# Kernel tuning notes

Hardware: AMD Instinct MI355X
Metric: run time of the kernel (lower is better)

## Reference

```python
import jax, jax.numpy as jnp
import numpy as np

N = 384          # item_num (text regions)
TD = 768         # text hidden (bert-base)
VD = 768         # vision hidden (vit-base)
CD = TD + VD     # commu_dim = 1536
FF = 2048        # TransformerEncoderLayer default dim_feedforward
H = 4            # nhead
L = 2            # num_layers per encoder
EPS = 1e-5


def _enc_params(key, d, scale=0.02):
    ks = jax.random.split(key, 6)
    return dict(
        qkv_w=jax.random.normal(ks[0], (L, 3 * d, d), jnp.float32) * scale,
        qkv_b=jnp.zeros((L, 3 * d), jnp.float32),
        out_w=jax.random.normal(ks[1], (L, d, d), jnp.float32) * scale,
        out_b=jnp.zeros((L, d), jnp.float32),
        ln1_s=jnp.ones((L, d), jnp.float32),
        ln1_b=jnp.zeros((L, d), jnp.float32),
        ff1_w=jax.random.normal(ks[2], (L, FF, d), jnp.float32) * scale,
        ff1_b=jnp.zeros((L, FF), jnp.float32),
        ff2_w=jax.random.normal(ks[3], (L, d, FF), jnp.float32) * scale,
        ff2_b=jnp.zeros((L, d), jnp.float32),
        ln2_s=jnp.ones((L, d), jnp.float32),
        ln2_b=jnp.zeros((L, d), jnp.float32),
    )


def setup_inputs() -> dict:
    key = jax.random.key(0)
    k = jax.random.split(key, 6)
    inp = {
        'text_emb': jax.random.normal(k[0], (N, TD), jnp.float32),
        'vision_emb': jax.random.normal(k[1], (N, VD), jnp.float32),
        'gt_matrix': jax.random.randint(k[2], (N, N), 0, 2, jnp.int32),
    }
    for pref, kk, d in (('t_', k[3], TD), ('c_', k[4], CD)):
        for name, v in _enc_params(kk, d).items():
            inp[pref + name] = v
    inp['lin_w'] = jax.random.normal(k[5], (2, 2 * CD), jnp.float32) * 0.02
    inp['lin_b'] = jnp.zeros((2,), jnp.float32)
    return inp


def _ln(x, s, b):
    m = jnp.mean(x, -1, keepdims=True)
    v = jnp.mean((x - m) ** 2, -1, keepdims=True)
    return (x - m) * jax.lax.rsqrt(v + EPS) * s + b


def _encoder(x, qkv_w, qkv_b, out_w, out_b, ln1_s, ln1_b,
             ff1_w, ff1_b, ff2_w, ff2_b, ln2_s, ln2_b):
    # PyTorch post-norm TransformerEncoder, relu activation, eval mode (no dropout)
    d = x.shape[-1]
    hd = d // H
    for l in range(qkv_w.shape[0]):
        qkv = x @ qkv_w[l].T + qkv_b[l]
        q, kk, v = jnp.split(qkv, 3, axis=-1)
        q = q.reshape(-1, H, hd)
        kk = kk.reshape(-1, H, hd)
        v = v.reshape(-1, H, hd)
        scores = jnp.einsum('qhd,khd->hqk', q, kk) / jnp.sqrt(jnp.float32(hd))
        attn = jax.nn.softmax(scores, -1)
        o = jnp.einsum('hqk,khd->qhd', attn, v).reshape(-1, d)
        x = _ln(x + o @ out_w[l].T + out_b[l], ln1_s[l], ln1_b[l])
        h = jax.nn.relu(x @ ff1_w[l].T + ff1_b[l]) @ ff2_w[l].T + ff2_b[l]
        x = _ln(x + h, ln2_s[l], ln2_b[l])
    return x


def reference(text_emb, vision_emb, gt_matrix,
              t_qkv_w, t_qkv_b, t_out_w, t_out_b, t_ln1_s, t_ln1_b,
              t_ff1_w, t_ff1_b, t_ff2_w, t_ff2_b, t_ln2_s, t_ln2_b,
              c_qkv_w, c_qkv_b, c_out_w, c_out_b, c_ln1_s, c_ln1_b,
              c_ff1_w, c_ff1_b, c_ff2_w, c_ff2_b, c_ln2_s, c_ln2_b,
              lin_w, lin_b):
    te = _encoder(text_emb, t_qkv_w, t_qkv_b, t_out_w, t_out_b, t_ln1_s, t_ln1_b,
                  t_ff1_w, t_ff1_b, t_ff2_w, t_ff2_b, t_ln2_s, t_ln2_b)
    all_emb = jnp.concatenate([te, vision_emb], axis=1)  # [N, CD]
    all_emb = _encoder(all_emb, c_qkv_w, c_qkv_b, c_out_w, c_out_b, c_ln1_s, c_ln1_b,
                       c_ff1_w, c_ff1_b, c_ff2_w, c_ff2_b, c_ln2_s, c_ln2_b)
    # organize(): linear(cat(e_i, e_j)) decomposes exactly as e_i@Wa^T + e_j@Wb^T + b,
    # avoiding the O(N^2 * 2*CD) pair tensor while computing identical math.
    a = all_emb @ lin_w[:, :CD].T + lin_b      # [N, 2]
    c = all_emb @ lin_w[:, CD:].T              # [N, 2]
    logits = a[:, None, :] + c[None, :, :]     # [N, N, 2]
    probs = jax.nn.softmax(logits, -1)         # self.activate(self.linear(...))
    # classificaiton_loss: sum_i CrossEntropyLoss(probs[i], gt[i])  (CE takes probs as logits)
    ls = jax.nn.log_softmax(probs, -1)
    cell = -jnp.take_along_axis(ls, gt_matrix[..., None].astype(jnp.int32), axis=-1)[..., 0]
    cls_loss = jnp.sum(jnp.mean(cell, axis=1))
    # enter_exit_loss over first N-1 items
    link = probs[:, :, 1]
    ee_loss = jnp.sum(jnp.abs(link.sum(1)[:-1] + link.sum(0)[:-1] - 1.0))
    return probs, cls_loss, ee_loss
```

## Files before the change

kernel.cpp:

```cpp
#include <hip/hip_runtime.h>
#include <hip/hip_bf16.h>
#include <math.h>

#define NTOK 384
#define HEADS 4

typedef __attribute__((ext_vector_type(8))) short bf16x8;
typedef __attribute__((ext_vector_type(4))) float f32x4;

__device__ __forceinline__ unsigned short f2b(float f) {
    union { float f; unsigned int u; } v; v.f = f;
    unsigned int r = (v.u + 0x7fff + ((v.u >> 16) & 1)) >> 16;
    return (unsigned short)r;
}

__device__ __forceinline__ void g2l16(const void* g, void* l) {
    __builtin_amdgcn_global_load_lds(
        (const __attribute__((address_space(1))) unsigned int*)g,
        (__attribute__((address_space(3))) unsigned int*)l, 16, 0, 0);
}

__device__ __forceinline__ void stage64(
    const unsigned short* __restrict__ g, int row0, int k0, int ld,
    char* region, int wid, int lane)
{
    int c = wid * 64 + lane;
    int row = c >> 2, p = c & 3;
    int kc = (p - (row >> 1)) & 3;
    g2l16(g + (long)(row0 + row) * ld + k0 + kc * 8,
          region + (wid * 64) * 16);
}

__device__ __forceinline__ void stage_tile(
    const unsigned short* __restrict__ A, const unsigned short* __restrict__ B,
    int row0, int col0, int k0, int lda, int ldb,
    char* buf, int wid, int lane)
{
    stage64(A, row0, k0,      lda, buf,         wid, lane);
    stage64(A, row0, k0 + 32, lda, buf +  4096, wid, lane);
    stage64(B, col0, k0,      ldb, buf +  8192, wid, lane);
    stage64(B, col0, k0 + 32, ldb, buf + 12288, wid, lane);
    __builtin_amdgcn_sched_barrier(0);
}

__global__ __launch_bounds__(256, 3) void gemm64(
    const unsigned short* __restrict__ A, const unsigned short* __restrict__ B,
    const float* __restrict__ bias, void* __restrict__ Cv,
    int K, int lda, int ldb, int ldc,
    long sA, long sB, long sC, int relu, int out_bf16)
{
    __shared__ char smem[3][16384];
    A += (long)blockIdx.z * sA;
    B += (long)blockIdx.z * sB;
    const int t = threadIdx.x, lane = t & 63, wid = t >> 6;
    const int wm = wid >> 1, wn = wid & 1;
    const int r16 = lane & 15, quad = lane >> 4;
    const int row0 = blockIdx.y * 64, col0 = blockIdx.x * 64;

    f32x4 acc[2][2] = {};
    const int NT = K >> 6;

    stage_tile(A, B, row0, col0, 0, lda, ldb, smem[0], wid, lane);
    if (NT > 1)
        stage_tile(A, B, row0, col0, 64, lda, ldb, smem[1], wid, lane);

    int cur = 0, sb = 2;
    for (int kt = 0; kt < NT; ++kt) {
        if (kt + 1 < NT) asm volatile("s_waitcnt vmcnt(4)" ::: "memory");
        else             asm volatile("s_waitcnt vmcnt(0) lgkmcnt(0)" ::: "memory");
        __builtin_amdgcn_s_barrier();
        if (kt + 2 < NT) {
            stage_tile(A, B, row0, col0, (kt + 2) * 64, lda, ldb,
                       smem[sb], wid, lane);
            sb = (sb == 2) ? 0 : sb + 1;
        }
        const char* cb = smem[cur];
        cur = (cur == 2) ? 0 : cur + 1;
        #pragma unroll
        for (int h = 0; h < 2; ++h) {
            bf16x8 af[2], bfv[2];
            #pragma unroll
            for (int rt = 0; rt < 2; ++rt) {
                int row = wm * 32 + rt * 16 + r16;
                int p = (quad + (row >> 1)) & 3;
                af[rt] = *reinterpret_cast<const bf16x8*>(
                    cb + h * 4096 + row * 64 + p * 16);
            }
            #pragma unroll
            for (int ct = 0; ct < 2; ++ct) {
                int col = wn * 32 + ct * 16 + r16;
                int p = (quad + (col >> 1)) & 3;
                bfv[ct] = *reinterpret_cast<const bf16x8*>(
                    cb + 8192 + h * 4096 + col * 64 + p * 16);
            }
            #pragma unroll
            for (int rt = 0; rt < 2; ++rt)
                #pragma unroll
                for (int ct = 0; ct < 2; ++ct)
                    acc[rt][ct] = __builtin_amdgcn_mfma_f32_16x16x32_bf16(
                        af[rt], bfv[ct], acc[rt][ct], 0, 0, 0);
        }
    }

    float* Cf = (float*)Cv;
    unsigned short* Cb = (unsigned short*)Cv;
    const long zoff = (long)blockIdx.z * sC;
    #pragma unroll
    for (int rt = 0; rt < 2; ++rt) {
        #pragma unroll
        for (int ct = 0; ct < 2; ++ct) {
            f32x4 v = acc[rt][ct];
            int col = col0 + wn * 32 + ct * 16 + r16;
            float bi = bias ? bias[col] : 0.f;
            #pragma unroll
            for (int i = 0; i < 4; ++i) {
                v[i] += bi;
                if (relu) v[i] = fmaxf(v[i], 0.f);
            }
            int rbase = row0 + wm * 32 + rt * 16 + quad * 4;
            if (out_bf16) {
                #pragma unroll
                for (int i = 0; i < 4; ++i)
                    Cb[zoff + (long)(rbase + i) * ldc + col] = f2b(v[i]);
            } else {
                #pragma unroll
                for (int i = 0; i < 4; ++i)
                    Cf[zoff + (long)(rbase + i) * ldc + col] = v[i];
            }
        }
    }
}

__device__ __forceinline__ void stage128(
    const unsigned short* __restrict__ g, int row0, int k0, int ld,
    char* region, int tid)
{
    int row = tid >> 2, p = tid & 3;
    int kc = (p - (row >> 1)) & 3;
    g2l16(g + (long)(row0 + row) * ld + k0 + kc * 8,
          region + ((tid >> 6) * 64) * 16);
}

__device__ __forceinline__ void stage_tile128(
    const unsigned short* __restrict__ A, const unsigned short* __restrict__ B,
    int row0, int col0, int k0, int lda, int ldb,
    char* buf, int tid)
{
    stage128(A, row0, k0,      lda, buf,          tid);
    stage128(A, row0, k0 + 32, lda, buf +  8192,  tid);
    stage128(B, col0, k0,      ldb, buf + 16384,  tid);
    stage128(B, col0, k0 + 32, ldb, buf + 24576,  tid);
    __builtin_amdgcn_sched_barrier(0);
}

__global__ __launch_bounds__(512, 1) void gemm128(
    const unsigned short* __restrict__ A, const unsigned short* __restrict__ B,
    const float* __restrict__ bias, void* __restrict__ Cv,
    int K, int lda, int ldb, int ldc, int relu, int out_bf16,
    unsigned short* __restrict__ vt, int dv2)
{
    __shared__ char smem[3][32768];
    const int t = threadIdx.x, lane = t & 63, wid = t >> 6;
    const int wm = wid >> 2, wn = wid & 3;
    const int r16 = lane & 15, quad = lane >> 4;
    const int row0 = blockIdx.y * 128, col0 = blockIdx.x * 128;

    f32x4 acc[4][2] = {};
    const int NT = K >> 6;

    stage_tile128(A, B, row0, col0, 0, lda, ldb, smem[0], t);
    if (NT > 1)
        stage_tile128(A, B, row0, col0, 64, lda, ldb, smem[1], t);

    int cur = 0, sb = 2;
    for (int kt = 0; kt < NT; ++kt) {
        if (kt + 1 < NT) asm volatile("s_waitcnt vmcnt(4)" ::: "memory");
        else             asm volatile("s_waitcnt vmcnt(0) lgkmcnt(0)" ::: "memory");
        __builtin_amdgcn_s_barrier();
        if (kt + 2 < NT) {
            stage_tile128(A, B, row0, col0, (kt + 2) * 64, lda, ldb,
                          smem[sb], t);
            sb = (sb == 2) ? 0 : sb + 1;
        }
        const char* cb = smem[cur];
        cur = (cur == 2) ? 0 : cur + 1;
        #pragma unroll
        for (int h = 0; h < 2; ++h) {
            bf16x8 af[4], bfv[2];
            #pragma unroll
            for (int rt = 0; rt < 4; ++rt) {
                int row = wm * 64 + rt * 16 + r16;
                int p = (quad + (row >> 1)) & 3;
                af[rt] = *reinterpret_cast<const bf16x8*>(
                    cb + h * 8192 + row * 64 + p * 16);
            }
            #pragma unroll
            for (int ct = 0; ct < 2; ++ct) {
                int col = wn * 32 + ct * 16 + r16;
                int p = (quad + (col >> 1)) & 3;
                bfv[ct] = *reinterpret_cast<const bf16x8*>(
                    cb + 16384 + h * 8192 + col * 64 + p * 16);
            }
            #pragma unroll
            for (int rt = 0; rt < 4; ++rt)
                #pragma unroll
                for (int ct = 0; ct < 2; ++ct)
                    acc[rt][ct] = __builtin_amdgcn_mfma_f32_16x16x32_bf16(
                        af[rt], bfv[ct], acc[rt][ct], 0, 0, 0);
        }
    }

    float* Cf = (float*)Cv;
    unsigned short* Cb = (unsigned short*)Cv;
    const int vwrite = (vt != nullptr) && (col0 >= dv2);
    #pragma unroll
    for (int rt = 0; rt < 4; ++rt) {
        #pragma unroll
        for (int ct = 0; ct < 2; ++ct) {
            f32x4 v = acc[rt][ct];
            int col = col0 + wn * 32 + ct * 16 + r16;
            float bi = bias ? bias[col] : 0.f;
            #pragma unroll
            for (int i = 0; i < 4; ++i) {
                v[i] += bi;
                if (relu) v[i] = fmaxf(v[i], 0.f);
            }
            int rbase = row0 + wm * 64 + rt * 16 + quad * 4;
            if (vwrite) {
                ushort4 p;
                p.x = f2b(v[0]); p.y = f2b(v[1]); p.z = f2b(v[2]); p.w = f2b(v[3]);
                *reinterpret_cast<ushort4*>(vt + (long)(col - dv2) * NTOK + rbase) = p;
            } else if (out_bf16) {
                #pragma unroll
                for (int i = 0; i < 4; ++i)
                    Cb[(long)(rbase + i) * ldc + col] = f2b(v[i]);
            } else {
                #pragma unroll
                for (int i = 0; i < 4; ++i)
                    Cf[(long)(rbase + i) * ldc + col] = v[i];
            }
        }
    }
}

#define WO0 0u
#define WO1 3538944u
#define WO2 4718592u
#define WO3 7864320u
#define WO4 11010048u
#define WO5 25165824u
#define WO6 29884416u
#define WO7 36175872u
#define WTOT 42467328u

__global__ __launch_bounds__(256) void convert_weights(
    const float* __restrict__ s0, const float* __restrict__ s1,
    const float* __restrict__ s2, const float* __restrict__ s3,
    const float* __restrict__ s4, const float* __restrict__ s5,
    const float* __restrict__ s6, const float* __restrict__ s7,
    unsigned short* __restrict__ dst)
{
    unsigned int e = (blockIdx.x * 256u + threadIdx.x) * 16u;
    if (e >= WTOT) return;
    const float* src; unsigned int local;
    if      (e < WO1) { src = s0; local = e - WO0; }
    else if (e < WO2) { src = s1; local = e - WO1; }
    else if (e < WO3) { src = s2; local = e - WO2; }
    else if (e < WO4) { src = s3; local = e - WO3; }
    else if (e < WO5) { src = s4; local = e - WO4; }
    else if (e < WO6) { src = s5; local = e - WO5; }
    else if (e < WO7) { src = s6; local = e - WO6; }
    else              { src = s7; local = e - WO7; }
    float4 v0 = *reinterpret_cast<const float4*>(src + local);
    float4 v1 = *reinterpret_cast<const float4*>(src + local + 4);
    float4 v2 = *reinterpret_cast<const float4*>(src + local + 8);
    float4 v3 = *reinterpret_cast<const float4*>(src + local + 12);
    uint4 o0, o1;
    o0.x = (unsigned)f2b(v0.x) | ((unsigned)f2b(v0.y) << 16);
    o0.y = (unsigned)f2b(v0.z) | ((unsigned)f2b(v0.w) << 16);
    o0.z = (unsigned)f2b(v1.x) | ((unsigned)f2b(v1.y) << 16);
    o0.w = (unsigned)f2b(v1.z) | ((unsigned)f2b(v1.w) << 16);
    o1.x = (unsigned)f2b(v2.x) | ((unsigned)f2b(v2.y) << 16);
    o1.y = (unsigned)f2b(v2.z) | ((unsigned)f2b(v2.w) << 16);
    o1.z = (unsigned)f2b(v3.x) | ((unsigned)f2b(v3.y) << 16);
    o1.w = (unsigned)f2b(v3.z) | ((unsigned)f2b(v3.w) << 16);
    *reinterpret_cast<uint4*>(dst + e) = o0;
    *reinterpret_cast<uint4*>(dst + e + 8) = o1;
}

__global__ __launch_bounds__(64) void softmax_rows(
    const float* __restrict__ S, unsigned short* __restrict__ P, float scale)
{
    const float* p = S + (long)blockIdx.x * NTOK;
    unsigned short* q = P + (long)blockIdx.x * NTOK;
    const int t = threadIdx.x;
    float vals[6];
    float vmax = -1e30f;
    #pragma unroll
    for (int i = 0; i < 6; ++i) {
        vals[i] = p[t + i * 64] * scale;
        vmax = fmaxf(vmax, vals[i]);
    }
    for (int off = 32; off; off >>= 1) vmax = fmaxf(vmax, __shfl_down(vmax, off));
    vmax = __shfl(vmax, 0);
    float sum = 0.f;
    #pragma unroll
    for (int i = 0; i < 6; ++i) { vals[i] = __expf(vals[i] - vmax); sum += vals[i]; }
    for (int off = 32; off; off >>= 1) sum += __shfl_down(sum, off);
    sum = __shfl(sum, 0);
    float inv = 1.f / sum;
    #pragma unroll
    for (int i = 0; i < 6; ++i) q[t + i * 64] = f2b(vals[i] * inv);
}

__global__ __launch_bounds__(256) void add_ln(
    float* __restrict__ x, unsigned short* __restrict__ xb,
    const float* __restrict__ y,
    const float* __restrict__ gb,
    const float* __restrict__ s, const float* __restrict__ b, int d)
{
    float* xr = x + (long)blockIdx.x * d;
    unsigned short* xbr = xb + (long)blockIdx.x * d;
    const float* yr = y + (long)blockIdx.x * d;
    const int t = threadIdx.x;
    float vv[6];
    float s1 = 0.f, s2 = 0.f;
    #pragma unroll
    for (int j = 0; j < 6; ++j) {
        int i = t + j * 256;
        if (j * 256 < d) {
            float v = xr[i] + gb[i] + yr[i];
            vv[j] = v;
            s1 += v; s2 += v * v;
        }
    }
    for (int off = 32; off; off >>= 1) { s1 += __shfl_down(s1, off); s2 += __shfl_down(s2, off); }
    __shared__ float r1[4], r2[4];
    int w = t >> 6;
    if ((t & 63) == 0) { r1[w] = s1; r2[w] = s2; }
    __syncthreads();
    if (t == 0) {
        float a = 0.f, c = 0.f;
        for (int i = 0; i < 4; ++i) { a += r1[i]; c += r2[i]; }
        r1[0] = a; r2[0] = c;
    }
    __syncthreads();
    float mean = r1[0] / d;
    float var = r2[0] / d - mean * mean;
    float rstd = rsqrtf(var + 1e-5f);
    #pragma unroll
    for (int j = 0; j < 6; ++j) {
        int i = t + j * 256;
        if (j * 256 < d) {
            float v = (vv[j] - mean) * rstd * s[i] + b[i];
            xr[i] = v;
            xbr[i] = f2b(v);
        }
    }
}

__global__ void initx_k(const float* __restrict__ src, float* __restrict__ dst,
                        unsigned short* __restrict__ dstb, int n)
{
    int i = blockIdx.x * blockDim.x + threadIdx.x;
    if (i < n) { float v = src[i]; dst[i] = v; dstb[i] = f2b(v); }
}

__global__ void concat_k(const float* __restrict__ te, const float* __restrict__ ve,
                         float* __restrict__ all, unsigned short* __restrict__ allb)
{
    int i = blockIdx.x * blockDim.x + threadIdx.x;
    if (i >= NTOK * 1536) return;
    int r = i / 1536, c = i % 1536;
    float v = (c < 768) ? te[r * 768 + c] : ve[r * 768 + (c - 768)];
    all[i] = v;
    allb[i] = f2b(v);
}

__global__ __launch_bounds__(256) void head_ac(
    const float* __restrict__ all, const float* __restrict__ lin_w,
    const float* __restrict__ lin_b, float* __restrict__ a, float* __restrict__ c)
{
    const int i = blockIdx.x, t = threadIdx.x;
    const float* xr = all + (long)i * 1536;
    float s0 = 0.f, s1 = 0.f, s2 = 0.f, s3 = 0.f;
    for (int e = t; e < 1536; e += 256) {
        float v = xr[e];
        s0 += v * lin_w[e];
        s1 += v * lin_w[3072 + e];
        s2 += v * lin_w[1536 + e];
        s3 += v * lin_w[4608 + e];
    }
    for (int off = 32; off; off >>= 1) {
        s0 += __shfl_down(s0, off); s1 += __shfl_down(s1, off);
        s2 += __shfl_down(s2, off); s3 += __shfl_down(s3, off);
    }
    __shared__ float r[4][4];
    int w = t >> 6;
    if ((t & 63) == 0) { r[0][w] = s0; r[1][w] = s1; r[2][w] = s2; r[3][w] = s3; }
    __syncthreads();
    if (t == 0) {
        float t0 = 0.f, t1 = 0.f, t2 = 0.f, t3 = 0.f;
        for (int k = 0; k < 4; ++k) { t0 += r[0][k]; t1 += r[1][k]; t2 += r[2][k]; t3 += r[3][k]; }
        a[i * 2 + 0] = t0 + lin_b[0];
        a[i * 2 + 1] = t1 + lin_b[1];
        c[i * 2 + 0] = t2;
        c[i * 2 + 1] = t3;
    }
}

__global__ __launch_bounds__(384) void head_probs(
    const float* __restrict__ a, const float* __restrict__ c,
    const int* __restrict__ gt, float* __restrict__ probs,
    float* __restrict__ rowsum, float* __restrict__ rowcell)
{
    const int i = blockIdx.x, j = threadIdx.x;
    float l0 = a[i * 2 + 0] + c[j * 2 + 0];
    float l1 = a[i * 2 + 1] + c[j * 2 + 1];
    float m = fmaxf(l0, l1);
    float e0 = __expf(l0 - m), e1 = __expf(l1 - m);
    float inv = 1.f / (e0 + e1);
    float p0 = e0 * inv, p1 = e1 * inv;
    long base = ((long)i * NTOK + j) * 2;
    probs[base] = p0;
    probs[base + 1] = p1;
    float m2 = fmaxf(p0, p1);
    float z = m2 + __logf(__expf(p0 - m2) + __expf(p1 - m2));
    int g = gt[i * NTOK + j];
    float cell = z - (g ? p1 : p0);
    float cs = cell, ps = p1;
    for (int off = 32; off; off >>= 1) { cs += __shfl_down(cs, off); ps += __shfl_down(ps, off); }
    __shared__ float rc[6], rs[6];
    int w = j >> 6;
    if ((j & 63) == 0) { rc[w] = cs; rs[w] = ps; }
    __syncthreads();
    if (j == 0) {
        float csum = 0.f, psum = 0.f;
        for (int k = 0; k < 6; ++k) { csum += rc[k]; psum += rs[k]; }
        rowcell[i] = csum * (1.f / NTOK);
        rowsum[i] = psum;
    }
}

__global__ __launch_bounds__(64) void colsum_k(const float* __restrict__ probs,
                                               float* __restrict__ colsum)
{
    const int j = blockIdx.x, t = threadIdx.x;
    float s = 0.f;
    for (int i = t; i < NTOK; i += 64)
        s += probs[((long)i * NTOK + j) * 2 + 1];
    for (int off = 32; off; off >>= 1) s += __shfl_down(s, off);
    if (t == 0) colsum[j] = s;
}

__global__ __launch_bounds__(384) void finalize_k(
    const float* __restrict__ rowcell, const float* __restrict__ rowsum,
    const float* __restrict__ colsum, float* __restrict__ out)
{
    const int t = threadIdx.x;
    float cls = rowcell[t];
    float ee = (t < NTOK - 1) ? fabsf(rowsum[t] + colsum[t] - 1.f) : 0.f;
    for (int off = 32; off; off >>= 1) { cls += __shfl_down(cls, off); ee += __shfl_down(ee, off); }
    __shared__ float rc[6], re[6];
    int w = t >> 6;
    if ((t & 63) == 0) { rc[w] = cls; re[w] = ee; }
    __syncthreads();
    if (t == 0) {
        float a = 0.f, b = 0.f;
        for (int k = 0; k < 6; ++k) { a += rc[k]; b += re[k]; }
        out[NTOK * NTOK * 2 + 0] = a;
        out[NTOK * NTOK * 2 + 1] = b;
    }
}

static void run_encoder(float* x, unsigned short* xb, int d,
                        const unsigned short* wq, const unsigned short* wo,
                        const unsigned short* w1, const unsigned short* w2,
                        const float* qkv_b, const float* out_b,
                        const float* ln1_s, const float* ln1_b,
                        const float* ff1_b, const float* ff2_b,
                        const float* ln2_s, const float* ln2_b,
                        unsigned short* qkvb, float* sc, unsigned short* attnb,
                        unsigned short* vtb, unsigned short* ob,
                        unsigned short* t1b, float* t2,
                        hipStream_t stream)
{
    const int dq = 3 * d;
    const int hd = d / HEADS;
    const float scale = 1.0f / sqrtf((float)hd);
    for (int l = 0; l < 2; ++l) {
        gemm128<<<dim3(dq / 128, NTOK / 128), 512, 0, stream>>>(
            xb, wq + (long)l * dq * d, qkv_b + l * dq, qkvb,
            d, d, d, dq, 0, 1, vtb, 2 * d);
        gemm64<<<dim3(6, 6, HEADS), 256, 0, stream>>>(
            qkvb, qkvb + d, nullptr, sc,
            hd, dq, dq, NTOK, (long)hd, (long)hd, (long)NTOK * NTOK, 0, 0);
        softmax_rows<<<HEADS * NTOK, 64, 0, stream>>>(sc, attnb, scale);
        gemm64<<<dim3(hd / 64, 6, HEADS), 256, 0, stream>>>(
            attnb, vtb, nullptr, ob,
            NTOK, NTOK, NTOK, d, (long)NTOK * NTOK, (long)hd * NTOK, (long)hd,
            0, 1);
        gemm128<<<dim3(d / 128, NTOK / 128), 512, 0, stream>>>(
            ob, wo + (long)l * d * d, nullptr, t2,
            d, d, d, d, 0, 0, nullptr, 0);
        add_ln<<<NTOK, 256, 0, stream>>>(x, xb, t2,
                                         out_b + l * d, ln1_s + l * d, ln1_b + l * d, d);
        gemm128<<<dim3(2048 / 128, NTOK / 128), 512, 0, stream>>>(
            xb, w1 + (long)l * 2048 * d, ff1_b + l * 2048, t1b,
            d, d, d, 2048, 1, 1, nullptr, 0);
        gemm128<<<dim3(d / 128, NTOK / 128), 512, 0, stream>>>(
            t1b, w2 + (long)l * d * 2048, nullptr, t2,
            2048, 2048, 2048, d, 0, 0, nullptr, 0);
        add_ln<<<NTOK, 256, 0, stream>>>(x, xb, t2,
                                         ff2_b + l * d, ln2_s + l * d, ln2_b + l * d, d);
    }
}

extern "C" void kernel_launch(void* const* d_in, const int* in_sizes, int n_in,
                              void* d_out, int out_size, void* d_ws, size_t ws_size,
                              hipStream_t stream)
{
    const float* text_emb   = (const float*)d_in[0];
    const float* vision_emb = (const float*)d_in[1];
    const int*   gt         = (const int*)  d_in[2];
    const float* t_qkv_w = (const float*)d_in[3];
    const float* t_qkv_b = (const float*)d_in[4];
    const float* t_out_w = (const float*)d_in[5];
    const float* t_out_b = (const float*)d_in[6];
    const float* t_ln1_s = (const float*)d_in[7];
    const float* t_ln1_b = (const float*)d_in[8];
    const float* t_ff1_w = (const float*)d_in[9];
    const float* t_ff1_b = (const float*)d_in[10];
    const float* t_ff2_w = (const float*)d_in[11];
    const float* t_ff2_b = (const float*)d_in[12];
    const float* t_ln2_s = (const float*)d_in[13];
    const float* t_ln2_b = (const float*)d_in[14];
    const float* c_qkv_w = (const float*)d_in[15];
    const float* c_qkv_b = (const float*)d_in[16];
    const float* c_out_w = (const float*)d_in[17];
    const float* c_out_b = (const float*)d_in[18];
    const float* c_ln1_s = (const float*)d_in[19];
    const float* c_ln1_b = (const float*)d_in[20];
    const float* c_ff1_w = (const float*)d_in[21];
    const float* c_ff1_b = (const float*)d_in[22];
    const float* c_ff2_w = (const float*)d_in[23];
    const float* c_ff2_b = (const float*)d_in[24];
    const float* c_ln2_s = (const float*)d_in[25];
    const float* c_ln2_b = (const float*)d_in[26];
    const float* lin_w   = (const float*)d_in[27];
    const float* lin_b   = (const float*)d_in[28];
    float* out = (float*)d_out;

    float* ws = (float*)d_ws;
    float* xt      = ws;
    float* all     = xt + 294912;
    float* t2      = all + 589824;
    float* sc      = t2 + 589824;
    float* abuf    = sc + 589824;
    float* cbuf    = abuf + 768;
    float* rowsum  = cbuf + 768;
    float* rowcell = rowsum + 384;
    float* colsum  = rowcell + 384;
    unsigned short* ub = (unsigned short*)(ws + 2067072);
    unsigned short* xtb   = ub;
    unsigned short* allb  = xtb + 294912;
    unsigned short* qkvb  = allb + 589824;
    unsigned short* attnb = qkvb + 1769472;
    unsigned short* vtb   = attnb + 589824;
    unsigned short* ob    = vtb + 589824;
    unsigned short* t1b   = ob + 589824;
    unsigned short* wb    = t1b + 786432;

    convert_weights<<<(WTOT / 16 + 255) / 256, 256, 0, stream>>>(
        t_qkv_w, t_out_w, t_ff1_w, t_ff2_w,
        c_qkv_w, c_out_w, c_ff1_w, c_ff2_w, wb);

    initx_k<<<(294912 + 255) / 256, 256, 0, stream>>>(text_emb, xt, xtb, 294912);
    run_encoder(xt, xtb, 768,
                wb + WO0, wb + WO1, wb + WO2, wb + WO3,
                t_qkv_b, t_out_b, t_ln1_s, t_ln1_b,
                t_ff1_b, t_ff2_b, t_ln2_s, t_ln2_b,
                qkvb, sc, attnb, vtb, ob, t1b, t2, stream);

    concat_k<<<(589824 + 255) / 256, 256, 0, stream>>>(xt, vision_emb, all, allb);
    run_encoder(all, allb, 1536,
                wb + WO4, wb + WO5, wb + WO6, wb + WO7,
                c_qkv_b, c_out_b, c_ln1_s, c_ln1_b,
                c_ff1_b, c_ff2_b, c_ln2_s, c_ln2_b,
                qkvb, sc, attnb, vtb, ob, t1b, t2, stream);

    head_ac<<<NTOK, 256, 0, stream>>>(all, lin_w, lin_b, abuf, cbuf);
    head_probs<<<NTOK, 384, 0, stream>>>(abuf, cbuf, gt, out, rowsum, rowcell);
    colsum_k<<<NTOK, 64, 0, stream>>>(out, colsum);
    finalize_k<<<1, 384, 0, stream>>>(rowcell, rowsum, colsum, out);
}
```

Before: 607.8 us.

## Fuse fp32 weight conversion into GEMM staging and drop the separate weight-convert kernel

Removes the convert_weights pre-pass that turned about 42M fp32 weights into bf16. The new 64x64-tile GEMM loads the fp32 weights straight into LDS with a swizzled layout and converts them to bf16 as it builds the MFMA fragments. This saves one full read and write of the weights, but each GEMM now reads twice as many weight bytes and does conversion work in the inner loop. The smaller tiles are meant to give more blocks at 384 rows, at the cost of less reuse per block.

```diff
diff --git a/kernel.cpp b/kernel.cpp
--- a/kernel.cpp
+++ b/kernel.cpp
@@ -12,6 +12,13 @@
     union { float f; unsigned int u; } v; v.f = f;
     unsigned int r = (v.u + 0x7fff + ((v.u >> 16) & 1)) >> 16;
     return (unsigned short)r;
+}
+
+__device__ __forceinline__ unsigned int cvt2(float a, float b) {
+    __hip_bfloat162 h = __float22bfloat162_rn(make_float2(a, b));
+    unsigned int u;
+    __builtin_memcpy(&u, &h, 4);
+    return u;
 }
 
 __device__ __forceinline__ void g2l16(const void* g, void* l) {
@@ -131,78 +138,92 @@
     }
 }
 
-__device__ __forceinline__ void stage128(
-    const unsigned short* __restrict__ g, int row0, int k0, int ld,
+__device__ __forceinline__ void stage32w(
+    const float* __restrict__ g, int col0, int k0, int ld,
     char* region, int tid)
 {
-    int row = tid >> 2, p = tid & 3;
-    int kc = (p - (row >> 1)) & 3;
-    g2l16(g + (long)(row0 + row) * ld + k0 + kc * 8,
-          region + ((tid >> 6) * 64) * 16);
-}
-
-__device__ __forceinline__ void stage_tile128(
-    const unsigned short* __restrict__ A, const unsigned short* __restrict__ B,
+    int wid = tid >> 6;
+    int row = tid >> 3, p = tid & 7;
+    int kc = (p - row) & 7;
+    g2l16(g + (long)(col0 + row) * ld + k0 + kc * 4,
+          region + wid * 1024);
+    int c2 = tid + 256;
+    int row2 = c2 >> 3, p2 = c2 & 7;
+    int kc2 = (p2 - row2) & 7;
+    g2l16(g + (long)(col0 + row2) * ld + k0 + kc2 * 4,
+          region + 4096 + wid * 1024);
+}
+
+__device__ __forceinline__ void stage_tile_w(
+    const unsigned short* __restrict__ A, const float* __restrict__ B,
     int row0, int col0, int k0, int lda, int ldb,
-    char* buf, int tid)
-{
-    stage128(A, row0, k0,      lda, buf,          tid);
-    stage128(A, row0, k0 + 32, lda, buf +  8192,  tid);
-    stage128(B, col0, k0,      ldb, buf + 16384,  tid);
-    stage128(B, col0, k0 + 32, ldb, buf + 24576,  tid);
+    char* buf, int wid, int lane, int tid)
+{
+    stage64(A, row0, k0,      lda, buf,        wid, lane);
+    stage64(A, row0, k0 + 32, lda, buf + 4096, wid, lane);
+    stage32w(B, col0, k0,      ldb, buf +  8192, tid);
+    stage32w(B, col0, k0 + 32, ldb, buf + 16384, tid);
     __builtin_amdgcn_sched_barrier(0);
 }
 
-__global__ __launch_bounds__(512, 1) void gemm128(
-    const unsigned short* __restrict__ A, const unsigned short* __restrict__ B,
+__global__ __launch_bounds__(256, 2) void gemm64w(
+    const unsigned short* __restrict__ A, const float* __restrict__ B,
     const float* __restrict__ bias, void* __restrict__ Cv,
     int K, int lda, int ldb, int ldc, int relu, int out_bf16,
     unsigned short* __restrict__ vt, int dv2)
 {
-    __shared__ char smem[3][32768];
+    __shared__ char smem[3][24576];
     const int t = threadIdx.x, lane = t & 63, wid = t >> 6;
-    const int wm = wid >> 2, wn = wid & 3;
+    const int wm = wid >> 1, wn = wid & 1;
     const int r16 = lane & 15, quad = lane >> 4;
-    const int row0 = blockIdx.y * 128, col0 = blockIdx.x * 128;
-
-    f32x4 acc[4][2] = {};
+    const int row0 = blockIdx.y * 64, col0 = blockIdx.x * 64;
+
+    f32x4 acc[2][2] = {};
     const int NT = K >> 6;
 
-    stage_tile128(A, B, row0, col0, 0, lda, ldb, smem[0], t);
+    stage_tile_w(A, B, row0, col0, 0, lda, ldb, smem[0], wid, lane, t);
     if (NT > 1)
-        stage_tile128(A, B, row0, col0, 64, lda, ldb, smem[1], t);
+        stage_tile_w(A, B, row0, col0, 64, lda, ldb, smem[1], wid, lane, t);
 
     int cur = 0, sb = 2;
     for (int kt = 0; kt < NT; ++kt) {
-        if (kt + 1 < NT) asm volatile("s_waitcnt vmcnt(4)" ::: "memory");
+        if (kt + 1 < NT) asm volatile("s_waitcnt vmcnt(6)" ::: "memory");
         else             asm volatile("s_waitcnt vmcnt(0) lgkmcnt(0)" ::: "memory");
         __builtin_amdgcn_s_barrier();
         if (kt + 2 < NT) {
-            stage_tile128(A, B, row0, col0, (kt + 2) * 64, lda, ldb,
-                          smem[sb], t);
+            stage_tile_w(A, B, row0, col0, (kt + 2) * 64, lda, ldb,
+                         smem[sb], wid, lane, t);
             sb = (sb == 2) ? 0 : sb + 1;
         }
         const char* cb = smem[cur];
         cur = (cur == 2) ? 0 : cur + 1;
         #pragma unroll
         for (int h = 0; h < 2; ++h) {
-            bf16x8 af[4], bfv[2];
-            #pragma unroll
-            for (int rt = 0; rt < 4; ++rt) {
-                int row = wm * 64 + rt * 16 + r16;
+            bf16x8 af[2], bfv[2];
+            #pragma unroll
+            for (int rt = 0; rt < 2; ++rt) {
+                int row = wm * 32 + rt * 16 + r16;
                 int p = (quad + (row >> 1)) & 3;
                 af[rt] = *reinterpret_cast<const bf16x8*>(
-                    cb + h * 8192 + row * 64 + p * 16);
+                    cb + h * 4096 + row * 64 + p * 16);
             }
             #pragma unroll
             for (int ct = 0; ct < 2; ++ct) {
-                int col = wn * 32 + ct * 16 + r16;
-                int p = (quad + (col >> 1)) & 3;
-                bfv[ct] = *reinterpret_cast<const bf16x8*>(
-                    cb + 16384 + h * 8192 + col * 64 + p * 16);
-            }
-            #pragma unroll
-            for (int rt = 0; rt < 4; ++rt)
+                int brow = wn * 32 + ct * 16 + r16;
+                const char* bb = cb + 8192 + h * 8192;
+                int p0 = ((quad << 1) + brow) & 7;
+                int p1 = ((quad << 1) + 1 + brow) & 7;
+                f32x4 u0 = *reinterpret_cast<const f32x4*>(bb + brow * 128 + p0 * 16);
+                f32x4 u1 = *reinterpret_cast<const f32x4*>(bb + brow * 128 + p1 * 16);
+                union { bf16x8 v; unsigned int u[4]; } pk;
+                pk.u[0] = cvt2(u0[0], u0[1]);
+                pk.u[1] = cvt2(u0[2], u0[3]);
+                pk.u[2] = cvt2(u1[0], u1[1]);
+                pk.u[3] = cvt2(u1[2], u1[3]);
+                bfv[ct] = pk.v;
+            }
+            #pragma unroll
+            for (int rt = 0; rt < 2; ++rt)
                 #pragma unroll
                 for (int ct = 0; ct < 2; ++ct)
                     acc[rt][ct] = __builtin_amdgcn_mfma_f32_16x16x32_bf16(
@@ -214,7 +235,7 @@
     unsigned short* Cb = (unsigned short*)Cv;
     const int vwrite = (vt != nullptr) && (col0 >= dv2);
     #pragma unroll
-    for (int rt = 0; rt < 4; ++rt) {
+    for (int rt = 0; rt < 2; ++rt) {
         #pragma unroll
         for (int ct = 0; ct < 2; ++ct) {
             f32x4 v = acc[rt][ct];
@@ -225,7 +246,7 @@
                 v[i] += bi;
                 if (relu) v[i] = fmaxf(v[i], 0.f);
             }
-            int rbase = row0 + wm * 64 + rt * 16 + quad * 4;
+            int rbase = row0 + wm * 32 + rt * 16 + quad * 4;
             if (vwrite) {
                 ushort4 p;
                 p.x = f2b(v[0]); p.y = f2b(v[1]); p.z = f2b(v[2]); p.w = f2b(v[3]);
@@ -241,51 +262,6 @@
             }
         }
     }
-}
-
-#define WO0 0u
-#define WO1 3538944u
-#define WO2 4718592u
-#define WO3 7864320u
-#define WO4 11010048u
-#define WO5 25165824u
-#define WO6 29884416u
-#define WO7 36175872u
-#define WTOT 42467328u
-
-__global__ __launch_bounds__(256) void convert_weights(
-    const float* __restrict__ s0, const float* __restrict__ s1,
-    const float* __restrict__ s2, const float* __restrict__ s3,
-    const float* __restrict__ s4, const float* __restrict__ s5,
-    const float* __restrict__ s6, const float* __restrict__ s7,
-    unsigned short* __restrict__ dst)
-{
-    unsigned int e = (blockIdx.x * 256u + threadIdx.x) * 16u;
-    if (e >= WTOT) return;
-    const float* src; unsigned int local;
-    if      (e < WO1) { src = s0; local = e - WO0; }
-    else if (e < WO2) { src = s1; local = e - WO1; }
-    else if (e < WO3) { src = s2; local = e - WO2; }
-    else if (e < WO4) { src = s3; local = e - WO3; }
-    else if (e < WO5) { src = s4; local = e - WO4; }
-    else if (e < WO6) { src = s5; local = e - WO5; }
-    else if (e < WO7) { src = s6; local = e - WO6; }
-    else              { src = s7; local = e - WO7; }
-    float4 v0 = *reinterpret_cast<const float4*>(src + local);
-    float4 v1 = *reinterpret_cast<const float4*>(src + local + 4);
-    float4 v2 = *reinterpret_cast<const float4*>(src + local + 8);
-    float4 v3 = *reinterpret_cast<const float4*>(src + local + 12);
-    uint4 o0, o1;
-    o0.x = (unsigned)f2b(v0.x) | ((unsigned)f2b(v0.y) << 16);
-    o0.y = (unsigned)f2b(v0.z) | ((unsigned)f2b(v0.w) << 16);
-    o0.z = (unsigned)f2b(v1.x) | ((unsigned)f2b(v1.y) << 16);
-    o0.w = (unsigned)f2b(v1.z) | ((unsigned)f2b(v1.w) << 16);
-    o1.x = (unsigned)f2b(v2.x) | ((unsigned)f2b(v2.y) << 16);
-    o1.y = (unsigned)f2b(v2.z) | ((unsigned)f2b(v2.w) << 16);
-    o1.z = (unsigned)f2b(v3.x) | ((unsigned)f2b(v3.y) << 16);
-    o1.w = (unsigned)f2b(v3.z) | ((unsigned)f2b(v3.w) << 16);
-    *reinterpret_cast<uint4*>(dst + e) = o0;
-    *reinterpret_cast<uint4*>(dst + e + 8) = o1;
 }
 
 __global__ __launch_bounds__(64) void softmax_rows(
@@ -474,8 +450,8 @@
 }
 
 static void run_encoder(float* x, unsigned short* xb, int d,
-                        const unsigned short* wq, const unsigned short* wo,
-                        const unsigned short* w1, const unsigned short* w2,
+                        const float* wq, const float* wo,
+                        const float* w1, const float* w2,
                         const float* qkv_b, const float* out_b,
                         const float* ln1_s, const float* ln1_b,
                         const float* ff1_b, const float* ff2_b,
@@ -489,7 +465,7 @@
     const int hd = d / HEADS;
     const float scale = 1.0f / sqrtf((float)hd);
     for (int l = 0; l < 2; ++l) {
-        gemm128<<<dim3(dq / 128, NTOK / 128), 512, 0, stream>>>(
+        gemm64w<<<dim3(dq / 64, 6), 256, 0, stream>>>(
             xb, wq + (long)l * dq * d, qkv_b + l * dq, qkvb,
             d, d, d, dq, 0, 1, vtb, 2 * d);
         gemm64<<<dim3(6, 6, HEADS), 256, 0, stream>>>(
@@ -500,15 +476,15 @@
             attnb, vtb, nullptr, ob,
             NTOK, NTOK, NTOK, d, (long)NTOK * NTOK, (long)hd * NTOK, (long)hd,
             0, 1);
-        gemm128<<<dim3(d / 128, NTOK / 128), 512, 0, stream>>>(
+        gemm64w<<<dim3(d / 64, 6), 256, 0, stream>>>(
             ob, wo + (long)l * d * d, nullptr, t2,
             d, d, d, d, 0, 0, nullptr, 0);
         add_ln<<<NTOK, 256, 0, stream>>>(x, xb, t2,
                                          out_b + l * d, ln1_s + l * d, ln1_b + l * d, d);
-        gemm128<<<dim3(2048 / 128, NTOK / 128), 512, 0, stream>>>(
+        gemm64w<<<dim3(2048 / 64, 6), 256, 0, stream>>>(
             xb, w1 + (long)l * 2048 * d, ff1_b + l * 2048, t1b,
             d, d, d, 2048, 1, 1, nullptr, 0);
-        gemm128<<<dim3(d / 128, NTOK / 128), 512, 0, stream>>>(
+        gemm64w<<<dim3(d / 64, 6), 256, 0, stream>>>(
             t1b, w2 + (long)l * d * 2048, nullptr, t2,
             2048, 2048, 2048, d, 0, 0, nullptr, 0);
         add_ln<<<NTOK, 256, 0, stream>>>(x, xb, t2,
@@ -569,22 +545,17 @@
     unsigned short* vtb   = attnb + 589824;
     unsigned short* ob    = vtb + 589824;
     unsigned short* t1b   = ob + 589824;
-    unsigned short* wb    = t1b + 786432;
-
-    convert_weights<<<(WTOT / 16 + 255) / 256, 256, 0, stream>>>(
-        t_qkv_w, t_out_w, t_ff1_w, t_ff2_w,
-        c_qkv_w, c_out_w, c_ff1_w, c_ff2_w, wb);
 
     initx_k<<<(294912 + 255) / 256, 256, 0, stream>>>(text_emb, xt, xtb, 294912);
     run_encoder(xt, xtb, 768,
-                wb + WO0, wb + WO1, wb + WO2, wb + WO3,
+                t_qkv_w, t_out_w, t_ff1_w, t_ff2_w,
                 t_qkv_b, t_out_b, t_ln1_s, t_ln1_b,
                 t_ff1_b, t_ff2_b, t_ln2_s, t_ln2_b,
                 qkvb, sc, attnb, vtb, ob, t1b, t2, stream);
 
     concat_k<<<(589824 + 255) / 256, 256, 0, stream>>>(xt, vision_emb, all, allb);
     run_encoder(all, allb, 1536,
-                wb + WO4, wb + WO5, wb + WO6, wb + WO7,
+                c_qkv_w, c_out_w, c_ff1_w, c_ff2_w,
                 c_qkv_b, c_out_b, c_ln1_s, c_ln1_b,
                 c_ff1_b, c_ff2_b, c_ln2_s, c_ln2_b,
                 qkvb, sc, attnb, vtb, ob, t1b, t2, stream);
```

New measurement: 550.9 us. 1.1x faster.
